# Performance work log

Measured on AMD Instinct MI355X. Metric: run time of the kernel, lower is better.

## Reference

```python
import jax, jax.numpy as jnp
import numpy as np

B, N, D, H, CH = 16, 2048, 2, 128, 32
NEG = -1e9


def setup_inputs() -> dict:
    key = jax.random.key(0)
    ks = jax.random.split(key, 24)
    u = lambda k, shape, fan_in: jax.random.uniform(k, shape, jnp.float32,
                                                    -1.0 / np.sqrt(fan_in), 1.0 / np.sqrt(fan_in))
    inp = {
        "features": jax.random.normal(ks[0], (B, N, D), jnp.float32),
        "adj": jax.random.randint(ks[1], (B, N, N), 0, 2, jnp.int32),
        "candidates": jax.random.randint(ks[2], (B, N), 0, 2, jnp.int32).at[:, 0].set(1),
        "action": jnp.zeros((B,), jnp.int32),
        # GCN encoder (3 layers)
        "W1": u(ks[3], (D, H), D), "b1": jnp.zeros((H,), jnp.float32),
        "W2": u(ks[4], (H, H), H), "b2": jnp.zeros((H,), jnp.float32),
        "W3": u(ks[5], (H, H), H), "b3": jnp.zeros((H,), jnp.float32),
        # learned machine state
        "machine_state": jax.random.uniform(ks[6], (H,), jnp.float32, -1.0, 1.0),
        # actor MLP: Linear(3H,H) -> ReLU -> Linear(H,H) -> ReLU -> Linear(H,1)
        "A1": u(ks[7], (3 * H, H), 3 * H), "ab1": u(ks[8], (H,), 3 * H),
        "A2": u(ks[9], (H, H), H), "ab2": u(ks[10], (H,), H),
        "A3": u(ks[11], (H, 1), H), "ab3": u(ks[12], (1,), H),
        # critic MLP: Linear(H,CH) -> ReLU -> Linear(CH,1)
        "C1": u(ks[13], (H, CH), H), "cb1": u(ks[14], (CH,), H),
        "C2": u(ks[15], (CH, 1), CH), "cb2": u(ks[16], (1,), CH),
    }
    return inp


def _gcn_propagation_matrix(adj):
    # Faithful to PyG GCNConv(add_self_loops=True) fed edges from dense_to_sparse
    # with edge attrs discarded (all weights 1).
    A = (adj != 0).astype(jnp.float32)                      # (B,N,N), A[b,j,i]: edge j->i
    A = jnp.maximum(A, jnp.eye(N, dtype=jnp.float32))       # add_remaining_self_loops
    deg = A.sum(axis=1)                                     # (B,N) incoming degree per target i
    dis = jax.lax.rsqrt(deg)                                # deg >= 1 due to self loops
    # S[b,j,i] = dis[j] * A[j,i] * dis[i]
    return dis[:, :, None] * A * dis[:, None, :]


def reference(features, adj, candidates, action,
              W1, b1, W2, b2, W3, b3, machine_state,
              A1, ab1, A2, ab2, A3, ab3, C1, cb1, C2, cb2):
    S = _gcn_propagation_matrix(adj)
    h = features
    for W, b in ((W1, b1), (W2, b2), (W3, b3)):
        # out[b,i,:] = sum_j S[b,j,i] * (h W)[b,j,:]
        h = jax.nn.relu(jnp.einsum('bji,bjd->bid', S, h @ W) + b)
    pool = h.mean(axis=1)                                   # (B,H) global mean pool

    concat = jnp.concatenate(
        [h,
         jnp.broadcast_to(pool[:, None, :], h.shape),
         jnp.broadcast_to(machine_state[None, None, :], h.shape)], axis=-1)  # (B,N,3H)
    a = jax.nn.relu(concat @ A1 + ab1)
    a = jax.nn.relu(a @ A2 + ab2)
    scores = ((a @ A3 + ab3)[..., 0]) * 10.0                # (B,N)

    probs_sm = jax.nn.softmax(scores, axis=1)               # softmax over jobs
    logits = jnp.where(candidates != 0, probs_sm, NEG)      # masked_fill(~candidates, -inf)
    logp = jax.nn.log_softmax(logits, axis=1)               # Categorical(logits=...)
    log_prob = jnp.take_along_axis(logp, action[:, None].astype(jnp.int32), axis=1)[:, 0]
    p = jnp.exp(logp)
    entropy = -(p * logp).sum(axis=1)

    value = jax.nn.relu(pool @ C1 + cb1) @ C2 + cb2         # (B,1)
    return action, log_prob, entropy, value
```

## Files before the change

### kernel.cpp

```cpp
#include <hip/hip_runtime.h>
#include <hip/hip_bf16.h>
#include <stdint.h>

#define B_  16
#define N_  2048
#define D_  2
#define H_  128
#define CH_ 32
#define NEG_ (-1e9f)

typedef __attribute__((ext_vector_type(8))) short bf16x8;
typedef __attribute__((ext_vector_type(4))) float f32x4;
typedef __attribute__((ext_vector_type(4))) int   v4i;
typedef unsigned short u16;
typedef signed char    i8;

__device__ inline u16 f2bf(float f){
    union { __hip_bfloat16 h; u16 u; } cv;
    cv.h = __float2bfloat16(f);
    return cv.u;
}
__device__ inline float bf2f(u16 v){ return __uint_as_float(((unsigned)v) << 16); }

__device__ inline void gld16b(const void* g, void* l){
    __builtin_amdgcn_global_load_lds(
        (const __attribute__((address_space(1))) unsigned int*)g,
        (__attribute__((address_space(3))) unsigned int*)l, 16, 0, 0);
}

__device__ inline float wredS(float v){
    #pragma unroll
    for (int o = 32; o; o >>= 1) v += __shfl_xor(v, o, 64);
    return v;
}
__device__ inline float wredM(float v){
    #pragma unroll
    for (int o = 32; o; o >>= 1) v = fmaxf(v, __shfl_xor(v, o, 64));
    return v;
}

__global__ __launch_bounds__(256) void k_prep(const int* __restrict__ adj,
                                              i8* __restrict__ ATi8,
                                              float* __restrict__ degF){
    int i0 = blockIdx.x * 64, j0 = blockIdx.y * 64, b = blockIdx.z;
    __shared__ i8 tile[64 * 80];
    __shared__ float degP[256];
    int t = threadIdx.x;
    const int* ap = adj + (size_t)b * N_ * N_;
    #pragma unroll
    for (int it = 0; it < 4; ++it){
        int jj = it * 16 + (t >> 4);
        int gi0 = (t & 15) * 4;
        int4 a4 = *(const int4*)&ap[(size_t)(j0 + jj) * N_ + i0 + gi0];
        int gj = j0 + jj;
        tile[(gi0 + 0) * 80 + jj] = (a4.x != 0 || gj == i0 + gi0 + 0) ? 1 : 0;
        tile[(gi0 + 1) * 80 + jj] = (a4.y != 0 || gj == i0 + gi0 + 1) ? 1 : 0;
        tile[(gi0 + 2) * 80 + jj] = (a4.z != 0 || gj == i0 + gi0 + 2) ? 1 : 0;
        tile[(gi0 + 3) * 80 + jj] = (a4.w != 0 || gj == i0 + gi0 + 3) ? 1 : 0;
    }
    __syncthreads();
    {
        int ii = t & 63, q = t >> 6;
        float s = 0.f;
        #pragma unroll
        for (int k = 0; k < 16; ++k) s += (float)tile[ii * 80 + q * 16 + k];
        degP[t] = s;
    }
    __syncthreads();
    if (t < 64){
        float s = degP[t] + degP[t + 64] + degP[t + 128] + degP[t + 192];
        atomicAdd(&degF[b * N_ + i0 + t], s);
    }
    i8* op = ATi8 + (size_t)b * N_ * N_;
    {
        int io = t >> 2, slot = (t & 3) * 16;
        *(uint4*)&op[(size_t)(i0 + io) * N_ + j0 + slot] = *(const uint4*)&tile[io * 80 + slot];
    }
}

__global__ __launch_bounds__(256) void k_misc(const float* __restrict__ degF,
                                              float* __restrict__ dis,
                                              const float* __restrict__ W2, u16* __restrict__ WT2,
                                              const float* __restrict__ W3, u16* __restrict__ WT3,
                                              const float* __restrict__ A1, u16* __restrict__ A1aT,
                                              const float* __restrict__ A2, u16* __restrict__ A2T){
    int bx = blockIdx.x;
    if (bx < 128){
        int i = bx * 256 + threadIdx.x;
        dis[i] = rsqrtf(degF[i]);
        return;
    }
    int q = (bx - 128) >> 6;
    const float* s; u16* d;
    switch (q){
        case 0: s = W2; d = WT2; break;
        case 1: s = W3; d = WT3; break;
        case 2: s = A1; d = A1aT; break;
        default: s = A2; d = A2T; break;
    }
    int idx = ((bx - 128) & 63) * 256 + threadIdx.x;
    int hp = idx >> 7, k = idx & 127;
    d[hp * 128 + k] = f2bf(s[k * 128 + hp]);
}

__global__ __launch_bounds__(256) void k_y1(const float* __restrict__ feat,
                                            const float* __restrict__ W1,
                                            const float* __restrict__ dis,
                                            u16* __restrict__ YT,
                                            int* __restrict__ absm){
    int t = threadIdx.x;
    int j = blockIdx.x * 256 + t;
    int hg = blockIdx.y * 8;
    int b = blockIdx.z;
    float f0 = feat[((size_t)b * N_ + j) * D_ + 0];
    float f1 = feat[((size_t)b * N_ + j) * D_ + 1];
    float dsc = dis[b * N_ + j];
    float lm = 0.f;
    #pragma unroll
    for (int hh = 0; hh < 8; ++hh){
        int h = hg + hh;
        float v = dsc * (f0 * W1[h] + f1 * W1[H_ + h]);
        lm = fmaxf(lm, fabsf(v));
        YT[(size_t)b * H_ * N_ + (size_t)h * N_ + j] = f2bf(v);
    }
    __shared__ float rmax[256];
    rmax[t] = lm;
    __syncthreads();
    if (t < 128) rmax[t] = fmaxf(rmax[t], rmax[t + 128]);
    __syncthreads();
    if (t < 64){
        float mv = wredM(fmaxf(rmax[t], rmax[t + 64]));
        if (t == 0) atomicMax(&absm[b], __float_as_int(mv));
    }
}

__global__ __launch_bounds__(256) void k_quant(const u16* __restrict__ Yb,
                                               const int* __restrict__ absm,
                                               i8* __restrict__ Yq){
    int idx = (blockIdx.x * 256 + threadIdx.x) * 8;
    int b = idx >> 18;
    float am = __int_as_float(absm[b]);
    float s = (am > 0.f) ? 126.f / am : 0.f;
    bf16x8 y = *(const bf16x8*)&Yb[idx];
    int q[8];
    #pragma unroll
    for (int e = 0; e < 8; ++e){
        float f = bf2f((u16)y[e]) * s;
        q[e] = (int)rintf(f);
    }
    unsigned lo = (q[0] & 255) | ((q[1] & 255) << 8) | ((q[2] & 255) << 16) | ((unsigned)(q[3] & 255) << 24);
    unsigned hi = (q[4] & 255) | ((q[5] & 255) << 8) | ((q[6] & 255) << 16) | ((unsigned)(q[7] & 255) << 24);
    *(uint2*)&Yq[idx] = make_uint2(lo, hi);
}

template<int MODE>
__global__ __launch_bounds__(256, 2) void k_layer(const i8* __restrict__ ATi8,
                                                  const i8* __restrict__ Yq,
                                                  const float* __restrict__ dis,
                                                  const float* __restrict__ bias,
                                                  const int* __restrict__ absmIn,
                                                  const u16* __restrict__ WT,
                                                  u16* __restrict__ Yout,
                                                  int* __restrict__ absmOut,
                                                  u16* __restrict__ h3,
                                                  float* __restrict__ poolF){
    int bid = blockIdx.x;
    int b = bid & 15, i0 = (bid >> 4) * 64;
    const i8* Ab = ATi8 + (size_t)b * N_ * N_ + (size_t)i0 * N_;
    const i8* Bb = Yq   + (size_t)b * H_ * N_;
    __shared__ __align__(16) i8 As[64 * 64];
    __shared__ __align__(16) i8 Bs[128 * 64];
    __shared__ __align__(16) u16 Hs[64 * 136];
    __shared__ __align__(16) u16 Ws[MODE == 0 ? 128 * 136 : 16];
    __shared__ float pmax[256];
    int t = threadIdx.x, w = t >> 6, lane = t & 63, quad = lane >> 4, l16 = lane & 15;
    int mr = w & 1, nc = w >> 1;

    float am = __int_as_float(absmIn[b]);
    float inv_s = am * (1.f / 126.f);

    if (MODE == 0){
        #pragma unroll
        for (int it = 0; it < 8; ++it){
            int e = it * 256 + t;
            int row = e >> 4, c8 = e & 15;
            *(uint4*)&Ws[row * 136 + c8 * 8] = *(const uint4*)&WT[row * 128 + c8 * 8];
        }
    }

    v4i acc[2][4];
    #pragma unroll
    for (int mt = 0; mt < 2; ++mt)
        #pragma unroll
        for (int nt = 0; nt < 4; ++nt) acc[mt][nt] = (v4i){0, 0, 0, 0};

    int srow = lane & 15;
    int sslot = ((lane >> 4) ^ (lane & 3)) * 16;
    int fxo = (quad ^ (l16 & 3)) * 256 + l16 * 16;

    for (int k0 = 0; k0 < N_; k0 += 64){
        #pragma unroll
        for (int it = 0; it < 3; ++it){
            int g = w * 3 + it;
            if (g < 4)
                gld16b(Ab + (size_t)(g * 16 + srow) * N_ + k0 + sslot, As + g * 1024);
            else
                gld16b(Bb + (size_t)((g - 4) * 16 + srow) * N_ + k0 + sslot, Bs + (g - 4) * 1024);
        }
        __syncthreads();
        v4i af[2];
        #pragma unroll
        for (int mt = 0; mt < 2; ++mt)
            af[mt] = *(const v4i*)&As[(mr * 2 + mt) * 1024 + fxo];
        #pragma unroll
        for (int nt = 0; nt < 4; ++nt){
            v4i bv = *(const v4i*)&Bs[(nc * 4 + nt) * 1024 + fxo];
            #pragma unroll
            for (int mt = 0; mt < 2; ++mt)
                acc[mt][nt] = __builtin_amdgcn_mfma_i32_16x16x64_i8(af[mt], bv, acc[mt][nt], 0, 0, 0);
        }
        __syncthreads();
    }

    #pragma unroll
    for (int mt = 0; mt < 2; ++mt)
        #pragma unroll
        for (int r = 0; r < 4; ++r){
            int m = mr * 32 + mt * 16 + quad * 4 + r;
            float dsc = dis[b * N_ + i0 + m];
            #pragma unroll
            for (int nt = 0; nt < 4; ++nt){
                int n = nc * 64 + nt * 16 + l16;
                float v = dsc * ((float)acc[mt][nt][r] * inv_s) + bias[n];
                Hs[m * 136 + n] = f2bf(v > 0.f ? v : 0.f);
            }
        }
    __syncthreads();

    if (MODE == 0){
        f32x4 a2[2][4];
        #pragma unroll
        for (int mt = 0; mt < 2; ++mt)
            #pragma unroll
            for (int nt = 0; nt < 4; ++nt) a2[mt][nt] = (f32x4){0.f, 0.f, 0.f, 0.f};
        #pragma unroll
        for (int kc = 0; kc < 4; ++kc){
            bf16x8 af[2];
            #pragma unroll
            for (int mt = 0; mt < 2; ++mt)
                af[mt] = *(const bf16x8*)&Hs[(mr * 32 + mt * 16 + l16) * 136 + kc * 32 + quad * 8];
            #pragma unroll
            for (int nt = 0; nt < 4; ++nt){
                bf16x8 bv = *(const bf16x8*)&Ws[(nc * 64 + nt * 16 + l16) * 136 + kc * 32 + quad * 8];
                #pragma unroll
                for (int mt = 0; mt < 2; ++mt)
                    a2[mt][nt] = __builtin_amdgcn_mfma_f32_16x16x32_bf16(af[mt], bv, a2[mt][nt], 0, 0, 0);
            }
        }
        __syncthreads();
        float lmax = 0.f;
        #pragma unroll
        for (int mt = 0; mt < 2; ++mt)
            #pragma unroll
            for (int r = 0; r < 4; ++r){
                int m = mr * 32 + mt * 16 + quad * 4 + r;
                float dsc = dis[b * N_ + i0 + m];
                #pragma unroll
                for (int nt = 0; nt < 4; ++nt){
                    float v = dsc * a2[mt][nt][r];
                    lmax = fmaxf(lmax, fabsf(v));
                    Hs[m * 136 + nc * 64 + nt * 16 + l16] = f2bf(v);
                }
            }
        pmax[t] = lmax;
        __syncthreads();
        size_t obase = (size_t)b * H_ * N_ + i0;
        int j = t & 63, hq = t >> 6;
        #pragma unroll 8
        for (int rep = 0; rep < 32; ++rep){
            int hrow = hq * 32 + rep;
            Yout[obase + (size_t)hrow * N_ + j] = Hs[j * 136 + hrow];
        }
        if (t < 64){
            float mv = fmaxf(fmaxf(pmax[t], pmax[t + 64]), fmaxf(pmax[t + 128], pmax[t + 192]));
            mv = wredM(mv);
            if (t == 0) atomicMax(&absmOut[b], __float_as_int(mv));
        }
    } else {
        #pragma unroll
        for (int rep = 0; rep < 4; ++rep){
            int e = rep * 256 + t;
            int row = e >> 4, c8 = e & 15;
            *(uint4*)&h3[((size_t)b * N_ + i0 + row) * H_ + c8 * 8] = *(const uint4*)&Hs[row * 136 + c8 * 8];
        }
        int n = t & 127, rq = t >> 7;
        float ps = 0.f;
        #pragma unroll 8
        for (int r = 0; r < 32; ++r) ps += bf2f(Hs[(rq * 32 + r) * 136 + n]);
        pmax[t] = ps;
        __syncthreads();
        if (t < 128)
            atomicAdd(&poolF[b * H_ + t], (pmax[t] + pmax[t + 128]) * (1.f / N_));
    }
}

__global__ __launch_bounds__(256) void k_cv(const float* __restrict__ poolF,
                                            const float* __restrict__ ms,
                                            const float* __restrict__ A1,
                                            const float* __restrict__ ab1,
                                            const float* __restrict__ C1,
                                            const float* __restrict__ cb1,
                                            const float* __restrict__ C2,
                                            const float* __restrict__ cb2,
                                            float* __restrict__ cvec,
                                            float* __restrict__ out){
    int b = blockIdx.x, t = threadIdx.x;
    __shared__ float pl[128], msl[128], v1[32];
    if (t < 128){ pl[t] = poolF[b * H_ + t]; msl[t] = ms[t]; }
    __syncthreads();
    if (t < 128){
        float c = ab1[t];
        for (int k = 0; k < 128; ++k)
            c += pl[k] * A1[(128 + k) * H_ + t] + msl[k] * A1[(256 + k) * H_ + t];
        cvec[b * H_ + t] = c;
    } else if (t < 160){
        int cc = t - 128;
        float v = cb1[cc];
        for (int k = 0; k < 128; ++k) v += pl[k] * C1[k * CH_ + cc];
        v1[cc] = v > 0.f ? v : 0.f;
    }
    __syncthreads();
    if (t == 0){
        float v = cb2[0];
        for (int c = 0; c < CH_; ++c) v += v1[c] * C2[c];
        out[48 + b] = v;
    }
}

__global__ __launch_bounds__(256) void k_actor(const u16* __restrict__ h3,
                                               const u16* __restrict__ A1aT,
                                               const u16* __restrict__ A2T,
                                               const float* __restrict__ cvec,
                                               const float* __restrict__ ab2,
                                               const float* __restrict__ A3,
                                               const float* __restrict__ ab3,
                                               float* __restrict__ scores){
    int b = blockIdx.x, i0 = blockIdx.y * 128;
    const u16* Ab = h3 + ((size_t)b * N_ + i0) * H_;
    __shared__ __align__(16) u16 As[128 * 72];
    __shared__ __align__(16) u16 Bs[128 * 72];
    __shared__ __align__(16) u16 M1[128 * 136];
    __shared__ float sLDS[128];
    int t = threadIdx.x, w = t >> 6, lane = t & 63, quad = lane >> 4, l16 = lane & 15;
    int sr = t >> 3, sc = (t & 7) * 8;
    f32x4 acc[2][8];
    #pragma unroll
    for (int mt = 0; mt < 2; ++mt)
        #pragma unroll
        for (int nt = 0; nt < 8; ++nt) acc[mt][nt] = (f32x4){0.f, 0.f, 0.f, 0.f};
    for (int k0 = 0; k0 < H_; k0 += 64){
        #pragma unroll
        for (int it = 0; it < 4; ++it){
            int r = sr + it * 32;
            *(uint4*)&As[r * 72 + sc] = *(const uint4*)&Ab[(size_t)r * H_ + k0 + sc];
            *(uint4*)&Bs[r * 72 + sc] = *(const uint4*)&A1aT[(size_t)r * H_ + k0 + sc];
        }
        __syncthreads();
        #pragma unroll
        for (int kc = 0; kc < 2; ++kc){
            bf16x8 af[2];
            #pragma unroll
            for (int mt = 0; mt < 2; ++mt)
                af[mt] = *(const bf16x8*)&As[(w * 32 + mt * 16 + l16) * 72 + kc * 32 + quad * 8];
            #pragma unroll
            for (int nt = 0; nt < 8; ++nt){
                bf16x8 bfr = *(const bf16x8*)&Bs[(nt * 16 + l16) * 72 + kc * 32 + quad * 8];
                #pragma unroll
                for (int mt = 0; mt < 2; ++mt)
                    acc[mt][nt] = __builtin_amdgcn_mfma_f32_16x16x32_bf16(af[mt], bfr, acc[mt][nt], 0, 0, 0);
            }
        }
        __syncthreads();
    }
    const float* cv = cvec + b * H_;
    #pragma unroll
    for (int mt = 0; mt < 2; ++mt)
        #pragma unroll
        for (int r = 0; r < 4; ++r){
            int m = w * 32 + mt * 16 + quad * 4 + r;
            #pragma unroll
            for (int nt = 0; nt < 8; ++nt){
                int n = nt * 16 + l16;
                float v = acc[mt][nt][r] + cv[n];
                M1[m * 136 + n] = f2bf(v > 0.f ? v : 0.f);
                acc[mt][nt][r] = 0.f;
            }
        }
    if (t < 128) sLDS[t] = 0.f;
    for (int k0 = 0; k0 < H_; k0 += 64){
        #pragma unroll
        for (int it = 0; it < 4; ++it){
            int r = sr + it * 32;
            *(uint4*)&Bs[r * 72 + sc] = *(const uint4*)&A2T[(size_t)r * H_ + k0 + sc];
        }
        __syncthreads();
        #pragma unroll
        for (int kc = 0; kc < 2; ++kc){
            bf16x8 af[2];
            #pragma unroll
            for (int mt = 0; mt < 2; ++mt)
                af[mt] = *(const bf16x8*)&M1[(w * 32 + mt * 16 + l16) * 136 + k0 + kc * 32 + quad * 8];
            #pragma unroll
            for (int nt = 0; nt < 8; ++nt){
                bf16x8 bfr = *(const bf16x8*)&Bs[(nt * 16 + l16) * 72 + kc * 32 + quad * 8];
                #pragma unroll
                for (int mt = 0; mt < 2; ++mt)
                    acc[mt][nt] = __builtin_amdgcn_mfma_f32_16x16x32_bf16(af[mt], bfr, acc[mt][nt], 0, 0, 0);
            }
        }
        __syncthreads();
    }
    #pragma unroll
    for (int mt = 0; mt < 2; ++mt)
        #pragma unroll
        for (int r = 0; r < 4; ++r){
            int m = w * 32 + mt * 16 + quad * 4 + r;
            float part = 0.f;
            #pragma unroll
            for (int nt = 0; nt < 8; ++nt){
                int n = nt * 16 + l16;
                float v = acc[mt][nt][r] + ab2[n];
                v = v > 0.f ? v : 0.f;
                part += v * A3[n];
            }
            atomicAdd(&sLDS[m], part);
        }
    __syncthreads();
    if (t < 128) scores[(size_t)b * N_ + i0 + t] = (sLDS[t] + ab3[0]) * 10.f;
}

__global__ __launch_bounds__(256) void k_sm(const float* __restrict__ scores,
                                            const int* __restrict__ cand,
                                            const int* __restrict__ action,
                                            float* __restrict__ out){
    int b = blockIdx.x, t = threadIdx.x;
    __shared__ float sc[N_];
    __shared__ float red[4];
    __shared__ float lps;
    const float* sp = scores + (size_t)b * N_;
    const int*   cp = cand   + (size_t)b * N_;
    float mx = -1e30f;
    for (int i = t; i < N_; i += 256){ float v = sp[i]; sc[i] = v; mx = fmaxf(mx, v); }
    mx = wredM(mx);
    if ((t & 63) == 0) red[t >> 6] = mx;
    __syncthreads();
    mx = fmaxf(fmaxf(red[0], red[1]), fmaxf(red[2], red[3]));
    __syncthreads();
    float se = 0.f;
    for (int i = t; i < N_; i += 256) se += expf(sc[i] - mx);
    se = wredS(se);
    if ((t & 63) == 0) red[t >> 6] = se;
    __syncthreads();
    float s1 = red[0] + red[1] + red[2] + red[3];
    __syncthreads();
    float inv = 1.f / s1;
    float m2 = -1e30f;
    for (int i = t; i < N_; i += 256){
        float p = expf(sc[i] - mx) * inv;
        sc[i] = p;
        if (cp[i] != 0) m2 = fmaxf(m2, p);
    }
    m2 = wredM(m2);
    if ((t & 63) == 0) red[t >> 6] = m2;
    __syncthreads();
    m2 = fmaxf(fmaxf(red[0], red[1]), fmaxf(red[2], red[3]));
    __syncthreads();
    float s2 = 0.f;
    for (int i = t; i < N_; i += 256) if (cp[i] != 0) s2 += expf(sc[i] - m2);
    s2 = wredS(s2);
    if ((t & 63) == 0) red[t >> 6] = s2;
    __syncthreads();
    float lse = m2 + logf(red[0] + red[1] + red[2] + red[3]);
    __syncthreads();
    int a = action[b];
    float ent = 0.f;
    for (int i = t; i < N_; i += 256){
        float lp = (cp[i] != 0 ? sc[i] : NEG_) - lse;
        float pe = expf(lp);
        ent -= pe * lp;
        if (i == a) lps = lp;
    }
    ent = wredS(ent);
    if ((t & 63) == 0) red[t >> 6] = ent;
    __syncthreads();
    if (t == 0){
        out[b]      = (float)a;
        out[16 + b] = lps;
        out[32 + b] = red[0] + red[1] + red[2] + red[3];
    }
}

extern "C" void kernel_launch(void* const* d_in, const int* in_sizes, int n_in,
                              void* d_out, int out_size, void* d_ws, size_t ws_size,
                              hipStream_t stream) {
    const float* feat = (const float*)d_in[0];
    const int*   adj  = (const int*)d_in[1];
    const int*   cand = (const int*)d_in[2];
    const int*   act  = (const int*)d_in[3];
    const float* W1   = (const float*)d_in[4];
    const float* b1   = (const float*)d_in[5];
    const float* W2   = (const float*)d_in[6];
    const float* b2   = (const float*)d_in[7];
    const float* W3   = (const float*)d_in[8];
    const float* b3   = (const float*)d_in[9];
    const float* ms   = (const float*)d_in[10];
    const float* A1   = (const float*)d_in[11];
    const float* ab1  = (const float*)d_in[12];
    const float* A2   = (const float*)d_in[13];
    const float* ab2  = (const float*)d_in[14];
    const float* A3   = (const float*)d_in[15];
    const float* ab3  = (const float*)d_in[16];
    const float* C1   = (const float*)d_in[17];
    const float* cb1  = (const float*)d_in[18];
    const float* C2   = (const float*)d_in[19];
    const float* cb2  = (const float*)d_in[20];
    float* out = (float*)d_out;

    char* w8 = (char*)d_ws;
    size_t off = 0;
    auto alloc = [&](size_t bytes){ void* p = w8 + off; off += (bytes + 255) & ~(size_t)255; return p; };
    i8*    ATi8  = (i8*)   alloc((size_t)B_ * N_ * N_);
    u16*   Yb16  = (u16*)  alloc((size_t)B_ * H_ * N_ * 2);
    i8*    Yi8A  = (i8*)   alloc((size_t)B_ * H_ * N_);
    i8*    Yi8B  = (i8*)   alloc((size_t)B_ * H_ * N_);
    u16*   hbuf  = (u16*)  alloc((size_t)B_ * N_ * H_ * 2);
    float* degF  = (float*)alloc((size_t)B_ * N_ * 4);
    float* poolF = (float*)alloc((size_t)B_ * H_ * 4);
    int*   absm  = (int*)  alloc(48 * 4);
    float* dis   = (float*)alloc((size_t)B_ * N_ * 4);
    float* cvec  = (float*)alloc((size_t)B_ * H_ * 4);
    float* scr   = (float*)alloc((size_t)B_ * N_ * 4);
    u16*   WT2   = (u16*)  alloc((size_t)H_ * H_ * 2);
    u16*   WT3   = (u16*)  alloc((size_t)H_ * H_ * 2);
    u16*   A1aT  = (u16*)  alloc((size_t)H_ * H_ * 2);
    u16*   A2T   = (u16*)  alloc((size_t)H_ * H_ * 2);

    hipMemsetAsync(degF, 0, (size_t)B_ * N_ * 4 + (size_t)B_ * H_ * 4 + 256, stream);

    k_prep<<<dim3(32, 32, 16), 256, 0, stream>>>(adj, ATi8, degF);
    k_misc<<<dim3(384), 256, 0, stream>>>(degF, dis, W2, WT2, W3, WT3, A1, A1aT, A2, A2T);
    k_y1  <<<dim3(8, 16, 16), 256, 0, stream>>>(feat, W1, dis, Yb16, absm + 0);
    k_quant<<<dim3(2048), 256, 0, stream>>>(Yb16, absm + 0, Yi8A);

    k_layer<0><<<dim3(512), 256, 0, stream>>>(ATi8, Yi8A, dis, b1, absm + 0,  WT2, Yb16, absm + 16, nullptr, nullptr);
    k_quant<<<dim3(2048), 256, 0, stream>>>(Yb16, absm + 16, Yi8B);
    k_layer<0><<<dim3(512), 256, 0, stream>>>(ATi8, Yi8B, dis, b2, absm + 16, WT3, Yb16, absm + 32, nullptr, nullptr);
    k_quant<<<dim3(2048), 256, 0, stream>>>(Yb16, absm + 32, Yi8A);
    k_layer<1><<<dim3(512), 256, 0, stream>>>(ATi8, Yi8A, dis, b3, absm + 32, nullptr, nullptr, nullptr, hbuf, poolF);

    k_cv  <<<dim3(16), 256, 0, stream>>>(poolF, ms, A1, ab1, C1, cb1, C2, cb2, cvec, out);
    k_actor<<<dim3(16, 16), 256, 0, stream>>>(hbuf, A1aT, A2T, cvec, ab2, A3, ab3, scr);
    k_sm  <<<dim3(16), 256, 0, stream>>>(scr, cand, act, out);
}
```

Baseline: 561.7 us.

## Fuse post-prep pipeline into one cooperative persistent kernel with grid syncs

Replaces the chain of separate launches after adjacency prep with a single cooperative kernel that runs every stage in phases separated by grid.sync, with a multi-launch fallback if the cooperative launch fails. Layer-1 input is now quantized directly with per-channel analytic bounds computed from feature maxima, which removes the bf16 intermediate and one quant pass. The separate dis buffer is dropped in favor of recomputing rsqrt(deg), and the second linear reads its weights straight from global memory instead of staging them in shared memory. The aim is to remove launch gaps and small kernels, at the cost of grid-sync overhead and possibly lower occupancy or weaker data reuse in the layer GEMM.

```diff
diff --git a/kernel.cpp b/kernel.cpp
--- a/kernel.cpp
+++ b/kernel.cpp
@@ -1,6 +1,9 @@
 #include <hip/hip_runtime.h>
 #include <hip/hip_bf16.h>
+#include <hip/hip_cooperative_groups.h>
 #include <stdint.h>
+
+namespace cg = cooperative_groups;
 
 #define B_  16
 #define N_  2048
@@ -78,115 +81,108 @@
     }
 }
 
-__global__ __launch_bounds__(256) void k_misc(const float* __restrict__ degF,
-                                              float* __restrict__ dis,
-                                              const float* __restrict__ W2, u16* __restrict__ WT2,
-                                              const float* __restrict__ W3, u16* __restrict__ WT3,
-                                              const float* __restrict__ A1, u16* __restrict__ A1aT,
-                                              const float* __restrict__ A2, u16* __restrict__ A2T){
-    int bx = blockIdx.x;
-    if (bx < 128){
-        int i = bx * 256 + threadIdx.x;
-        dis[i] = rsqrtf(degF[i]);
-        return;
-    }
-    int q = (bx - 128) >> 6;
-    const float* s; u16* d;
-    switch (q){
-        case 0: s = W2; d = WT2; break;
-        case 1: s = W3; d = WT3; break;
-        case 2: s = A1; d = A1aT; break;
-        default: s = A2; d = A2T; break;
-    }
-    int idx = ((bx - 128) & 63) * 256 + threadIdx.x;
-    int hp = idx >> 7, k = idx & 127;
-    d[hp * 128 + k] = f2bf(s[k * 128 + hp]);
-}
-
-__global__ __launch_bounds__(256) void k_y1(const float* __restrict__ feat,
-                                            const float* __restrict__ W1,
-                                            const float* __restrict__ dis,
-                                            u16* __restrict__ YT,
-                                            int* __restrict__ absm){
-    int t = threadIdx.x;
-    int j = blockIdx.x * 256 + t;
-    int hg = blockIdx.y * 8;
-    int b = blockIdx.z;
-    float f0 = feat[((size_t)b * N_ + j) * D_ + 0];
-    float f1 = feat[((size_t)b * N_ + j) * D_ + 1];
-    float dsc = dis[b * N_ + j];
-    float lm = 0.f;
-    #pragma unroll
-    for (int hh = 0; hh < 8; ++hh){
-        int h = hg + hh;
-        float v = dsc * (f0 * W1[h] + f1 * W1[H_ + h]);
-        lm = fmaxf(lm, fabsf(v));
-        YT[(size_t)b * H_ * N_ + (size_t)h * N_ + j] = f2bf(v);
-    }
-    __shared__ float rmax[256];
-    rmax[t] = lm;
-    __syncthreads();
-    if (t < 128) rmax[t] = fmaxf(rmax[t], rmax[t + 128]);
-    __syncthreads();
-    if (t < 64){
-        float mv = wredM(fmaxf(rmax[t], rmax[t + 64]));
-        if (t == 0) atomicMax(&absm[b], __float_as_int(mv));
-    }
-}
-
-__global__ __launch_bounds__(256) void k_quant(const u16* __restrict__ Yb,
-                                               const int* __restrict__ absm,
-                                               i8* __restrict__ Yq){
-    int idx = (blockIdx.x * 256 + threadIdx.x) * 8;
-    int b = idx >> 18;
-    float am = __int_as_float(absm[b]);
-    float s = (am > 0.f) ? 126.f / am : 0.f;
-    bf16x8 y = *(const bf16x8*)&Yb[idx];
-    int q[8];
-    #pragma unroll
-    for (int e = 0; e < 8; ++e){
-        float f = bf2f((u16)y[e]) * s;
-        q[e] = (int)rintf(f);
-    }
-    unsigned lo = (q[0] & 255) | ((q[1] & 255) << 8) | ((q[2] & 255) << 16) | ((unsigned)(q[3] & 255) << 24);
-    unsigned hi = (q[4] & 255) | ((q[5] & 255) << 8) | ((q[6] & 255) << 16) | ((unsigned)(q[7] & 255) << 24);
-    *(uint2*)&Yq[idx] = make_uint2(lo, hi);
-}
-
-template<int MODE>
-__global__ __launch_bounds__(256, 2) void k_layer(const i8* __restrict__ ATi8,
-                                                  const i8* __restrict__ Yq,
-                                                  const float* __restrict__ dis,
-                                                  const float* __restrict__ bias,
-                                                  const int* __restrict__ absmIn,
-                                                  const u16* __restrict__ WT,
-                                                  u16* __restrict__ Yout,
-                                                  int* __restrict__ absmOut,
-                                                  u16* __restrict__ h3,
-                                                  float* __restrict__ poolF){
-    int bid = blockIdx.x;
-    int b = bid & 15, i0 = (bid >> 4) * 64;
-    const i8* Ab = ATi8 + (size_t)b * N_ * N_ + (size_t)i0 * N_;
-    const i8* Bb = Yq   + (size_t)b * H_ * N_;
-    __shared__ __align__(16) i8 As[64 * 64];
-    __shared__ __align__(16) i8 Bs[128 * 64];
-    __shared__ __align__(16) u16 Hs[64 * 136];
-    __shared__ __align__(16) u16 Ws[MODE == 0 ? 128 * 136 : 16];
-    __shared__ float pmax[256];
-    int t = threadIdx.x, w = t >> 6, lane = t & 63, quad = lane >> 4, l16 = lane & 15;
+struct MegaArgs {
+    const float *feat; const int *cand; const int *act;
+    const float *W1, *b1, *W2, *b2, *W3, *b3, *ms;
+    const float *A1, *ab1, *A2, *ab2, *A3, *ab3;
+    const float *C1, *cb1, *C2, *cb2;
+    const i8 *ATi8;
+    float *degF, *poolF; int *absm;
+    float *m01, *invs1, *cvec, *scr;
+    u16 *Yb16, *hbuf, *WT2, *WT3, *A1aT, *A2T;
+    i8 *Yq1, *Yq2;
+    float *out;
+};
+
+__device__ void dev_p1(const MegaArgs& a, int bx, int t, char* smem){
+    if (bx < 16){
+        int b = bx;
+        float lm0 = 0.f, lm1 = 0.f;
+        #pragma unroll
+        for (int it = 0; it < 8; ++it){
+            int j = it * 256 + t;
+            float dsj = rsqrtf(a.degF[b * N_ + j]);
+            lm0 = fmaxf(lm0, dsj * fabsf(a.feat[((size_t)b * N_ + j) * 2 + 0]));
+            lm1 = fmaxf(lm1, dsj * fabsf(a.feat[((size_t)b * N_ + j) * 2 + 1]));
+        }
+        float* r0 = (float*)smem;
+        float* r1 = (float*)(smem + 1024);
+        r0[t] = lm0; r1[t] = lm1;
+        __syncthreads();
+        if (t < 128){ r0[t] = fmaxf(r0[t], r0[t + 128]); r1[t] = fmaxf(r1[t], r1[t + 128]); }
+        __syncthreads();
+        if (t < 64){
+            float m0 = wredM(fmaxf(r0[t], r0[t + 64]));
+            float m1 = wredM(fmaxf(r1[t], r1[t + 64]));
+            if (t == 0){ a.m01[b * 2] = m0; a.m01[b * 2 + 1] = m1; }
+        }
+        __syncthreads();
+    } else if (bx < 272){
+        int q = (bx - 16) >> 6;
+        const float* s; u16* d;
+        switch (q){
+            case 0: s = a.W2; d = a.WT2; break;
+            case 1: s = a.W3; d = a.WT3; break;
+            case 2: s = a.A1; d = a.A1aT; break;
+            default: s = a.A2; d = a.A2T; break;
+        }
+        int idx = ((bx - 16) & 63) * 256 + t;
+        int hp = idx >> 7, k = idx & 127;
+        d[hp * 128 + k] = f2bf(s[k * 128 + hp]);
+    }
+}
+
+__device__ void dev_y1q(const MegaArgs& a, int vb, int t){
+    int b = vb & 15, seg = vb >> 4;
+    float m0 = a.m01[b * 2], m1 = a.m01[b * 2 + 1];
+    int j0 = t * 8;
+    float4 f4[4];
+    #pragma unroll
+    for (int k = 0; k < 4; ++k)
+        f4[k] = *(const float4*)&a.feat[((size_t)b * N_ + j0) * 2 + k * 4];
+    const float* ff = (const float*)f4;
+    float dsj[8];
+    #pragma unroll
+    for (int e = 0; e < 8; ++e) dsj[e] = rsqrtf(a.degF[b * N_ + j0 + e]);
+    #pragma unroll
+    for (int hh = 0; hh < 4; ++hh){
+        int h = seg * 4 + hh;
+        float w0 = a.W1[h], w1 = a.W1[H_ + h];
+        float bound = m0 * fabsf(w0) + m1 * fabsf(w1);
+        float s = (bound > 0.f) ? 126.f / bound : 0.f;
+        if (t == 0) a.invs1[b * H_ + h] = bound * (1.f / 126.f);
+        int q[8];
+        #pragma unroll
+        for (int e = 0; e < 8; ++e){
+            float v = dsj[e] * (ff[2 * e] * w0 + ff[2 * e + 1] * w1);
+            q[e] = (int)rintf(v * s);
+        }
+        unsigned lo = (q[0] & 255) | ((q[1] & 255) << 8) | ((q[2] & 255) << 16) | ((unsigned)(q[3] & 255) << 24);
+        unsigned hi = (q[4] & 255) | ((q[5] & 255) << 8) | ((q[6] & 255) << 16) | ((unsigned)(q[7] & 255) << 24);
+        *(uint2*)&a.Yq1[(size_t)b * H_ * N_ + (size_t)h * N_ + j0] = make_uint2(lo, hi);
+    }
+}
+
+template<int PER_N, int MODE>
+__device__ void layer_phase(const MegaArgs& a, int vbid, int t,
+                            const i8* __restrict__ Yq,
+                            const float* __restrict__ bias,
+                            const int* __restrict__ absmIn,
+                            const u16* __restrict__ WTg,
+                            u16* __restrict__ Yout, int* __restrict__ absmBase,
+                            char* smem){
+    int b = vbid & 15, i0 = (vbid >> 4) * 64;
+    const i8* Ab = a.ATi8 + (size_t)b * N_ * N_ + (size_t)i0 * N_;
+    const i8* Bb = Yq + (size_t)b * H_ * N_;
+    i8*  As = (i8*)smem;
+    i8*  Bs = (i8*)(smem + 4096);
+    u16* Hs = (u16*)(smem + 12288);
+    float* pmax = (float*)(smem + 29696);
+    int w = t >> 6, lane = t & 63, quad = lane >> 4, l16 = lane & 15;
     int mr = w & 1, nc = w >> 1;
 
-    float am = __int_as_float(absmIn[b]);
-    float inv_s = am * (1.f / 126.f);
-
-    if (MODE == 0){
-        #pragma unroll
-        for (int it = 0; it < 8; ++it){
-            int e = it * 256 + t;
-            int row = e >> 4, c8 = e & 15;
-            *(uint4*)&Ws[row * 136 + c8 * 8] = *(const uint4*)&WT[row * 128 + c8 * 8];
-        }
-    }
+    float inv_s = PER_N ? 0.f : __int_as_float(absmIn[b]) * (1.f / 126.f);
+    const float* invN = PER_N ? (a.invs1 + b * H_) : nullptr;
 
     v4i acc[2][4];
     #pragma unroll
@@ -227,11 +223,12 @@
         #pragma unroll
         for (int r = 0; r < 4; ++r){
             int m = mr * 32 + mt * 16 + quad * 4 + r;
-            float dsc = dis[b * N_ + i0 + m];
+            float dsc = rsqrtf(a.degF[b * N_ + i0 + m]);
             #pragma unroll
             for (int nt = 0; nt < 4; ++nt){
                 int n = nc * 64 + nt * 16 + l16;
-                float v = dsc * ((float)acc[mt][nt][r] * inv_s) + bias[n];
+                float z = (float)acc[mt][nt][r] * (PER_N ? invN[n] : inv_s);
+                float v = dsc * z + bias[n];
                 Hs[m * 136 + n] = f2bf(v > 0.f ? v : 0.f);
             }
         }
@@ -251,7 +248,7 @@
                 af[mt] = *(const bf16x8*)&Hs[(mr * 32 + mt * 16 + l16) * 136 + kc * 32 + quad * 8];
             #pragma unroll
             for (int nt = 0; nt < 4; ++nt){
-                bf16x8 bv = *(const bf16x8*)&Ws[(nc * 64 + nt * 16 + l16) * 136 + kc * 32 + quad * 8];
+                bf16x8 bv = *(const bf16x8*)&WTg[(size_t)(nc * 64 + nt * 16 + l16) * H_ + kc * 32 + quad * 8];
                 #pragma unroll
                 for (int mt = 0; mt < 2; ++mt)
                     a2[mt][nt] = __builtin_amdgcn_mfma_f32_16x16x32_bf16(af[mt], bv, a2[mt][nt], 0, 0, 0);
@@ -264,7 +261,7 @@
             #pragma unroll
             for (int r = 0; r < 4; ++r){
                 int m = mr * 32 + mt * 16 + quad * 4 + r;
-                float dsc = dis[b * N_ + i0 + m];
+                float dsc = rsqrtf(a.degF[b * N_ + i0 + m]);
                 #pragma unroll
                 for (int nt = 0; nt < 4; ++nt){
                     float v = dsc * a2[mt][nt][r];
@@ -284,14 +281,14 @@
         if (t < 64){
             float mv = fmaxf(fmaxf(pmax[t], pmax[t + 64]), fmaxf(pmax[t + 128], pmax[t + 192]));
             mv = wredM(mv);
-            if (t == 0) atomicMax(&absmOut[b], __float_as_int(mv));
+            if (t == 0) atomicMax(absmBase + b, __float_as_int(mv));
         }
     } else {
         #pragma unroll
         for (int rep = 0; rep < 4; ++rep){
             int e = rep * 256 + t;
             int row = e >> 4, c8 = e & 15;
-            *(uint4*)&h3[((size_t)b * N_ + i0 + row) * H_ + c8 * 8] = *(const uint4*)&Hs[row * 136 + c8 * 8];
+            *(uint4*)&a.hbuf[((size_t)b * N_ + i0 + row) * H_ + c8 * 8] = *(const uint4*)&Hs[row * 136 + c8 * 8];
         }
         int n = t & 127, rq = t >> 7;
         float ps = 0.f;
@@ -300,155 +297,120 @@
         pmax[t] = ps;
         __syncthreads();
         if (t < 128)
-            atomicAdd(&poolF[b * H_ + t], (pmax[t] + pmax[t + 128]) * (1.f / N_));
-    }
-}
-
-__global__ __launch_bounds__(256) void k_cv(const float* __restrict__ poolF,
-                                            const float* __restrict__ ms,
-                                            const float* __restrict__ A1,
-                                            const float* __restrict__ ab1,
-                                            const float* __restrict__ C1,
-                                            const float* __restrict__ cb1,
-                                            const float* __restrict__ C2,
-                                            const float* __restrict__ cb2,
-                                            float* __restrict__ cvec,
-                                            float* __restrict__ out){
-    int b = blockIdx.x, t = threadIdx.x;
-    __shared__ float pl[128], msl[128], v1[32];
-    if (t < 128){ pl[t] = poolF[b * H_ + t]; msl[t] = ms[t]; }
+            atomicAdd(&a.poolF[b * H_ + t], (pmax[t] + pmax[t + 128]) * (1.f / N_));
+    }
+    __syncthreads();
+}
+
+__device__ void dev_quant(const MegaArgs& a, int stage, int vb, int t){
+    const int* am = a.absm + stage * 16;
+    i8* dst = stage ? a.Yq1 : a.Yq2;
+    int idx = vb * 256 + t;
+    #pragma unroll
+    for (int it = 0; it < 4; ++it){
+        int pos = (it * 131072 + idx) * 8;
+        int b = pos >> 18;
+        float m = __int_as_float(am[b]);
+        float s = (m > 0.f) ? 126.f / m : 0.f;
+        bf16x8 y = *(const bf16x8*)&a.Yb16[pos];
+        int q[8];
+        #pragma unroll
+        for (int e = 0; e < 8; ++e) q[e] = (int)rintf(bf2f((u16)y[e]) * s);
+        unsigned lo = (q[0] & 255) | ((q[1] & 255) << 8) | ((q[2] & 255) << 16) | ((unsigned)(q[3] & 255) << 24);
+        unsigned hi = (q[4] & 255) | ((q[5] & 255) << 8) | ((q[6] & 255) << 16) | ((unsigned)(q[7] & 255) << 24);
+        *(uint2*)&dst[pos] = make_uint2(lo, hi);
+    }
+}
+
+__device__ void dev_cv(const MegaArgs& a, int b, int t, char* smem){
+    float* pl  = (float*)smem;
+    float* msl = (float*)(smem + 512);
+    float* v1  = (float*)(smem + 1024);
+    if (t < 128){ pl[t] = a.poolF[b * H_ + t]; msl[t] = a.ms[t]; }
     __syncthreads();
     if (t < 128){
-        float c = ab1[t];
+        float c = a.ab1[t];
         for (int k = 0; k < 128; ++k)
-            c += pl[k] * A1[(128 + k) * H_ + t] + msl[k] * A1[(256 + k) * H_ + t];
-        cvec[b * H_ + t] = c;
+            c += pl[k] * a.A1[(128 + k) * H_ + t] + msl[k] * a.A1[(256 + k) * H_ + t];
+        a.cvec[b * H_ + t] = c;
     } else if (t < 160){
         int cc = t - 128;
-        float v = cb1[cc];
-        for (int k = 0; k < 128; ++k) v += pl[k] * C1[k * CH_ + cc];
+        float v = a.cb1[cc];
+        for (int k = 0; k < 128; ++k) v += pl[k] * a.C1[k * CH_ + cc];
         v1[cc] = v > 0.f ? v : 0.f;
     }
     __syncthreads();
     if (t == 0){
-        float v = cb2[0];
-        for (int c = 0; c < CH_; ++c) v += v1[c] * C2[c];
-        out[48 + b] = v;
-    }
-}
-
-__global__ __launch_bounds__(256) void k_actor(const u16* __restrict__ h3,
-                                               const u16* __restrict__ A1aT,
-                                               const u16* __restrict__ A2T,
-                                               const float* __restrict__ cvec,
-                                               const float* __restrict__ ab2,
-                                               const float* __restrict__ A3,
-                                               const float* __restrict__ ab3,
-                                               float* __restrict__ scores){
-    int b = blockIdx.x, i0 = blockIdx.y * 128;
-    const u16* Ab = h3 + ((size_t)b * N_ + i0) * H_;
-    __shared__ __align__(16) u16 As[128 * 72];
-    __shared__ __align__(16) u16 Bs[128 * 72];
-    __shared__ __align__(16) u16 M1[128 * 136];
-    __shared__ float sLDS[128];
-    int t = threadIdx.x, w = t >> 6, lane = t & 63, quad = lane >> 4, l16 = lane & 15;
-    int sr = t >> 3, sc = (t & 7) * 8;
-    f32x4 acc[2][8];
-    #pragma unroll
-    for (int mt = 0; mt < 2; ++mt)
-        #pragma unroll
-        for (int nt = 0; nt < 8; ++nt) acc[mt][nt] = (f32x4){0.f, 0.f, 0.f, 0.f};
-    for (int k0 = 0; k0 < H_; k0 += 64){
-        #pragma unroll
-        for (int it = 0; it < 4; ++it){
-            int r = sr + it * 32;
-            *(uint4*)&As[r * 72 + sc] = *(const uint4*)&Ab[(size_t)r * H_ + k0 + sc];
-            *(uint4*)&Bs[r * 72 + sc] = *(const uint4*)&A1aT[(size_t)r * H_ + k0 + sc];
-        }
-        __syncthreads();
-        #pragma unroll
-        for (int kc = 0; kc < 2; ++kc){
-            bf16x8 af[2];
-            #pragma unroll
-            for (int mt = 0; mt < 2; ++mt)
-                af[mt] = *(const bf16x8*)&As[(w * 32 + mt * 16 + l16) * 72 + kc * 32 + quad * 8];
-            #pragma unroll
-            for (int nt = 0; nt < 8; ++nt){
-                bf16x8 bfr = *(const bf16x8*)&Bs[(nt * 16 + l16) * 72 + kc * 32 + quad * 8];
-                #pragma unroll
-                for (int mt = 0; mt < 2; ++mt)
-                    acc[mt][nt] = __builtin_amdgcn_mfma_f32_16x16x32_bf16(af[mt], bfr, acc[mt][nt], 0, 0, 0);
-            }
-        }
-        __syncthreads();
-    }
-    const float* cv = cvec + b * H_;
-    #pragma unroll
-    for (int mt = 0; mt < 2; ++mt)
-        #pragma unroll
-        for (int r = 0; r < 4; ++r){
-            int m = w * 32 + mt * 16 + quad * 4 + r;
-            #pragma unroll
-            for (int nt = 0; nt < 8; ++nt){
-                int n = nt * 16 + l16;
-                float v = acc[mt][nt][r] + cv[n];
-                M1[m * 136 + n] = f2bf(v > 0.f ? v : 0.f);
-                acc[mt][nt][r] = 0.f;
-            }
-        }
-    if (t < 128) sLDS[t] = 0.f;
-    for (int k0 = 0; k0 < H_; k0 += 64){
-        #pragma unroll
-        for (int it = 0; it < 4; ++it){
-            int r = sr + it * 32;
-            *(uint4*)&Bs[r * 72 + sc] = *(const uint4*)&A2T[(size_t)r * H_ + k0 + sc];
-        }
-        __syncthreads();
-        #pragma unroll
-        for (int kc = 0; kc < 2; ++kc){
-            bf16x8 af[2];
-            #pragma unroll
-            for (int mt = 0; mt < 2; ++mt)
-                af[mt] = *(const bf16x8*)&M1[(w * 32 + mt * 16 + l16) * 136 + k0 + kc * 32 + quad * 8];
-            #pragma unroll
-            for (int nt = 0; nt < 8; ++nt){
-                bf16x8 bfr = *(const bf16x8*)&Bs[(nt * 16 + l16) * 72 + kc * 32 + quad * 8];
-                #pragma unroll
-                for (int mt = 0; mt < 2; ++mt)
-                    acc[mt][nt] = __builtin_amdgcn_mfma_f32_16x16x32_bf16(af[mt], bfr, acc[mt][nt], 0, 0, 0);
-            }
-        }
-        __syncthreads();
-    }
-    #pragma unroll
-    for (int mt = 0; mt < 2; ++mt)
-        #pragma unroll
-        for (int r = 0; r < 4; ++r){
-            int m = w * 32 + mt * 16 + quad * 4 + r;
-            float part = 0.f;
-            #pragma unroll
-            for (int nt = 0; nt < 8; ++nt){
-                int n = nt * 16 + l16;
-                float v = acc[mt][nt][r] + ab2[n];
-                v = v > 0.f ? v : 0.f;
-                part += v * A3[n];
-            }
-            atomicAdd(&sLDS[m], part);
-        }
-    __syncthreads();
-    if (t < 128) scores[(size_t)b * N_ + i0 + t] = (sLDS[t] + ab3[0]) * 10.f;
-}
-
-__global__ __launch_bounds__(256) void k_sm(const float* __restrict__ scores,
-                                            const int* __restrict__ cand,
-                                            const int* __restrict__ action,
-                                            float* __restrict__ out){
-    int b = blockIdx.x, t = threadIdx.x;
-    __shared__ float sc[N_];
-    __shared__ float red[4];
-    __shared__ float lps;
-    const float* sp = scores + (size_t)b * N_;
-    const int*   cp = cand   + (size_t)b * N_;
+        float v = a.cb2[0];
+        for (int c = 0; c < CH_; ++c) v += v1[c] * a.C2[c];
+        a.out[48 + b] = v;
+    }
+    __syncthreads();
+}
+
+__device__ void dev_actor(const MegaArgs& a, int vbid, int t, char* smem){
+    int b = vbid & 15, i0 = (vbid >> 4) * 64;
+    const u16* Ab = a.hbuf + ((size_t)b * N_ + i0) * H_;
+    u16* M1 = (u16*)smem;
+    int w = t >> 6, lane = t & 63, quad = lane >> 4, l16 = lane & 15;
+    f32x4 acc[8];
+    #pragma unroll
+    for (int nt = 0; nt < 8; ++nt) acc[nt] = (f32x4){0.f, 0.f, 0.f, 0.f};
+    #pragma unroll
+    for (int kc = 0; kc < 4; ++kc){
+        bf16x8 af = *(const bf16x8*)&Ab[(size_t)(w * 16 + l16) * H_ + kc * 32 + quad * 8];
+        #pragma unroll
+        for (int nt = 0; nt < 8; ++nt){
+            bf16x8 bv = *(const bf16x8*)&a.A1aT[(size_t)(nt * 16 + l16) * H_ + kc * 32 + quad * 8];
+            acc[nt] = __builtin_amdgcn_mfma_f32_16x16x32_bf16(af, bv, acc[nt], 0, 0, 0);
+        }
+    }
+    const float* cv = a.cvec + b * H_;
+    #pragma unroll
+    for (int r = 0; r < 4; ++r){
+        int m = w * 16 + quad * 4 + r;
+        #pragma unroll
+        for (int nt = 0; nt < 8; ++nt){
+            int n = nt * 16 + l16;
+            float v = acc[nt][r] + cv[n];
+            M1[m * 136 + n] = f2bf(v > 0.f ? v : 0.f);
+            acc[nt][r] = 0.f;
+        }
+    }
+    #pragma unroll
+    for (int kc = 0; kc < 4; ++kc){
+        bf16x8 af = *(const bf16x8*)&M1[(w * 16 + l16) * 136 + kc * 32 + quad * 8];
+        #pragma unroll
+        for (int nt = 0; nt < 8; ++nt){
+            bf16x8 bv = *(const bf16x8*)&a.A2T[(size_t)(nt * 16 + l16) * H_ + kc * 32 + quad * 8];
+            acc[nt] = __builtin_amdgcn_mfma_f32_16x16x32_bf16(af, bv, acc[nt], 0, 0, 0);
+        }
+    }
+    float ab3v = a.ab3[0];
+    #pragma unroll
+    for (int r = 0; r < 4; ++r){
+        int m = w * 16 + quad * 4 + r;
+        float part = 0.f;
+        #pragma unroll
+        for (int nt = 0; nt < 8; ++nt){
+            int n = nt * 16 + l16;
+            float v = acc[nt][r] + a.ab2[n];
+            v = v > 0.f ? v : 0.f;
+            part += v * a.A3[n];
+        }
+        #pragma unroll
+        for (int o = 1; o < 16; o <<= 1) part += __shfl_xor(part, o, 64);
+        if (l16 == 0) a.scr[(size_t)b * N_ + i0 + m] = (part + ab3v) * 10.f;
+    }
+    __syncthreads();
+}
+
+__device__ void dev_sm(const MegaArgs& a, int b, int t, char* smem){
+    float* sc  = (float*)smem;
+    float* red = (float*)(smem + 8192);
+    float* lps = (float*)(smem + 8256);
+    const float* sp = a.scr + (size_t)b * N_;
+    const int*   cp = a.cand + (size_t)b * N_;
     float mx = -1e30f;
     for (int i = t; i < N_; i += 256){ float v = sp[i]; sc[i] = v; mx = fmaxf(mx, v); }
     mx = wredM(mx);
@@ -482,22 +444,87 @@
     __syncthreads();
     float lse = m2 + logf(red[0] + red[1] + red[2] + red[3]);
     __syncthreads();
-    int a = action[b];
+    int ac = a.act[b];
     float ent = 0.f;
     for (int i = t; i < N_; i += 256){
         float lp = (cp[i] != 0 ? sc[i] : NEG_) - lse;
         float pe = expf(lp);
         ent -= pe * lp;
-        if (i == a) lps = lp;
+        if (i == ac) *lps = lp;
     }
     ent = wredS(ent);
     if ((t & 63) == 0) red[t >> 6] = ent;
     __syncthreads();
     if (t == 0){
-        out[b]      = (float)a;
-        out[16 + b] = lps;
-        out[32 + b] = red[0] + red[1] + red[2] + red[3];
-    }
+        a.out[b]      = (float)ac;
+        a.out[16 + b] = *lps;
+        a.out[32 + b] = red[0] + red[1] + red[2] + red[3];
+    }
+}
+
+__global__ __launch_bounds__(256, 2) void k_mega(MegaArgs a){
+    cg::grid_group grid = cg::this_grid();
+    __shared__ __align__(16) char smem[30720];
+    int bid = blockIdx.x, t = threadIdx.x, G = gridDim.x;
+
+    for (int bx = bid; bx < 272; bx += G) dev_p1(a, bx, t, smem);
+    grid.sync();
+    for (int vb = bid; vb < 512; vb += G) dev_y1q(a, vb, t);
+    grid.sync();
+    for (int vb = bid; vb < 512; vb += G)
+        layer_phase<1, 0>(a, vb, t, a.Yq1, a.b1, nullptr, a.WT2, a.Yb16, a.absm, smem);
+    grid.sync();
+    for (int vb = bid; vb < 512; vb += G) dev_quant(a, 0, vb, t);
+    grid.sync();
+    for (int vb = bid; vb < 512; vb += G)
+        layer_phase<0, 0>(a, vb, t, a.Yq2, a.b2, a.absm, a.WT3, a.Yb16, a.absm + 16, smem);
+    grid.sync();
+    for (int vb = bid; vb < 512; vb += G) dev_quant(a, 1, vb, t);
+    grid.sync();
+    for (int vb = bid; vb < 512; vb += G)
+        layer_phase<0, 1>(a, vb, t, a.Yq1, a.b3, a.absm + 16, nullptr, nullptr, nullptr, smem);
+    grid.sync();
+    if (bid < 16) dev_cv(a, bid, t, smem);
+    grid.sync();
+    for (int vb = bid; vb < 512; vb += G) dev_actor(a, vb, t, smem);
+    grid.sync();
+    if (bid < 16) dev_sm(a, bid, t, smem);
+}
+
+__global__ __launch_bounds__(256) void f_p1(MegaArgs a){
+    __shared__ __align__(16) char sm[2048];
+    dev_p1(a, blockIdx.x, threadIdx.x, sm);
+}
+__global__ __launch_bounds__(256) void f_y1q(MegaArgs a){
+    dev_y1q(a, blockIdx.x, threadIdx.x);
+}
+__global__ __launch_bounds__(256, 2) void f_l1(MegaArgs a){
+    __shared__ __align__(16) char sm[30720];
+    layer_phase<1, 0>(a, blockIdx.x, threadIdx.x, a.Yq1, a.b1, nullptr, a.WT2, a.Yb16, a.absm, sm);
+}
+__global__ __launch_bounds__(256, 2) void f_l2(MegaArgs a){
+    __shared__ __align__(16) char sm[30720];
+    layer_phase<0, 0>(a, blockIdx.x, threadIdx.x, a.Yq2, a.b2, a.absm, a.WT3, a.Yb16, a.absm + 16, sm);
+}
+__global__ __launch_bounds__(256, 2) void f_l3(MegaArgs a){
+    __shared__ __align__(16) char sm[30720];
+    layer_phase<0, 1>(a, blockIdx.x, threadIdx.x, a.Yq1, a.b3, a.absm + 16, nullptr, nullptr, nullptr, sm);
+}
+template<int S>
+__global__ __launch_bounds__(256) void f_q(MegaArgs a){
+    dev_quant(a, S, blockIdx.x, threadIdx.x);
+}
+__global__ __launch_bounds__(256) void f_cv(MegaArgs a){
+    __shared__ __align__(16) char sm[2048];
+    dev_cv(a, blockIdx.x, threadIdx.x, sm);
+}
+__global__ __launch_bounds__(256) void f_actor(MegaArgs a){
+    __shared__ __align__(16) char sm[17408];
+    dev_actor(a, blockIdx.x, threadIdx.x, sm);
+}
+__global__ __launch_bounds__(256) void f_sm(MegaArgs a){
+    __shared__ __align__(16) char sm[8320];
+    dev_sm(a, blockIdx.x, threadIdx.x, sm);
 }
 
 extern "C" void kernel_launch(void* const* d_in, const int* in_sizes, int n_in,
@@ -505,39 +532,20 @@
                               hipStream_t stream) {
     const float* feat = (const float*)d_in[0];
     const int*   adj  = (const int*)d_in[1];
-    const int*   cand = (const int*)d_in[2];
-    const int*   act  = (const int*)d_in[3];
-    const float* W1   = (const float*)d_in[4];
-    const float* b1   = (const float*)d_in[5];
-    const float* W2   = (const float*)d_in[6];
-    const float* b2   = (const float*)d_in[7];
-    const float* W3   = (const float*)d_in[8];
-    const float* b3   = (const float*)d_in[9];
-    const float* ms   = (const float*)d_in[10];
-    const float* A1   = (const float*)d_in[11];
-    const float* ab1  = (const float*)d_in[12];
-    const float* A2   = (const float*)d_in[13];
-    const float* ab2  = (const float*)d_in[14];
-    const float* A3   = (const float*)d_in[15];
-    const float* ab3  = (const float*)d_in[16];
-    const float* C1   = (const float*)d_in[17];
-    const float* cb1  = (const float*)d_in[18];
-    const float* C2   = (const float*)d_in[19];
-    const float* cb2  = (const float*)d_in[20];
-    float* out = (float*)d_out;
 
     char* w8 = (char*)d_ws;
     size_t off = 0;
     auto alloc = [&](size_t bytes){ void* p = w8 + off; off += (bytes + 255) & ~(size_t)255; return p; };
     i8*    ATi8  = (i8*)   alloc((size_t)B_ * N_ * N_);
     u16*   Yb16  = (u16*)  alloc((size_t)B_ * H_ * N_ * 2);
-    i8*    Yi8A  = (i8*)   alloc((size_t)B_ * H_ * N_);
-    i8*    Yi8B  = (i8*)   alloc((size_t)B_ * H_ * N_);
+    i8*    Yq1   = (i8*)   alloc((size_t)B_ * H_ * N_);
+    i8*    Yq2   = (i8*)   alloc((size_t)B_ * H_ * N_);
     u16*   hbuf  = (u16*)  alloc((size_t)B_ * N_ * H_ * 2);
     float* degF  = (float*)alloc((size_t)B_ * N_ * 4);
     float* poolF = (float*)alloc((size_t)B_ * H_ * 4);
-    int*   absm  = (int*)  alloc(48 * 4);
-    float* dis   = (float*)alloc((size_t)B_ * N_ * 4);
+    int*   absm  = (int*)  alloc(256);
+    float* m01   = (float*)alloc(32 * 4);
+    float* invs1 = (float*)alloc((size_t)B_ * H_ * 4);
     float* cvec  = (float*)alloc((size_t)B_ * H_ * 4);
     float* scr   = (float*)alloc((size_t)B_ * N_ * 4);
     u16*   WT2   = (u16*)  alloc((size_t)H_ * H_ * 2);
@@ -548,17 +556,43 @@
     hipMemsetAsync(degF, 0, (size_t)B_ * N_ * 4 + (size_t)B_ * H_ * 4 + 256, stream);
 
     k_prep<<<dim3(32, 32, 16), 256, 0, stream>>>(adj, ATi8, degF);
-    k_misc<<<dim3(384), 256, 0, stream>>>(degF, dis, W2, WT2, W3, WT3, A1, A1aT, A2, A2T);
-    k_y1  <<<dim3(8, 16, 16), 256, 0, stream>>>(feat, W1, dis, Yb16, absm + 0);
-    k_quant<<<dim3(2048), 256, 0, stream>>>(Yb16, absm + 0, Yi8A);
-
-    k_layer<0><<<dim3(512), 256, 0, stream>>>(ATi8, Yi8A, dis, b1, absm + 0,  WT2, Yb16, absm + 16, nullptr, nullptr);
-    k_quant<<<dim3(2048), 256, 0, stream>>>(Yb16, absm + 16, Yi8B);
-    k_layer<0><<<dim3(512), 256, 0, stream>>>(ATi8, Yi8B, dis, b2, absm + 16, WT3, Yb16, absm + 32, nullptr, nullptr);
-    k_quant<<<dim3(2048), 256, 0, stream>>>(Yb16, absm + 32, Yi8A);
-    k_layer<1><<<dim3(512), 256, 0, stream>>>(ATi8, Yi8A, dis, b3, absm + 32, nullptr, nullptr, nullptr, hbuf, poolF);
-
-    k_cv  <<<dim3(16), 256, 0, stream>>>(poolF, ms, A1, ab1, C1, cb1, C2, cb2, cvec, out);
-    k_actor<<<dim3(16, 16), 256, 0, stream>>>(hbuf, A1aT, A2T, cvec, ab2, A3, ab3, scr);
-    k_sm  <<<dim3(16), 256, 0, stream>>>(scr, cand, act, out);
-}
+
+    MegaArgs ma;
+    ma.feat = feat; ma.cand = (const int*)d_in[2]; ma.act = (const int*)d_in[3];
+    ma.W1 = (const float*)d_in[4];  ma.b1 = (const float*)d_in[5];
+    ma.W2 = (const float*)d_in[6];  ma.b2 = (const float*)d_in[7];
+    ma.W3 = (const float*)d_in[8];  ma.b3 = (const float*)d_in[9];
+    ma.ms = (const float*)d_in[10];
+    ma.A1 = (const float*)d_in[11]; ma.ab1 = (const float*)d_in[12];
+    ma.A2 = (const float*)d_in[13]; ma.ab2 = (const float*)d_in[14];
+    ma.A3 = (const float*)d_in[15]; ma.ab3 = (const float*)d_in[16];
+    ma.C1 = (const float*)d_in[17]; ma.cb1 = (const float*)d_in[18];
+    ma.C2 = (const float*)d_in[19]; ma.cb2 = (const float*)d_in[20];
+    ma.ATi8 = ATi8; ma.degF = degF; ma.poolF = poolF; ma.absm = absm;
+    ma.m01 = m01; ma.invs1 = invs1; ma.cvec = cvec; ma.scr = scr;
+    ma.Yb16 = Yb16; ma.hbuf = hbuf; ma.WT2 = WT2; ma.WT3 = WT3;
+    ma.A1aT = A1aT; ma.A2T = A2T; ma.Yq1 = Yq1; ma.Yq2 = Yq2;
+    ma.out = (float*)d_out;
+
+    void* params[] = { &ma };
+    hipError_t ce = hipLaunchCooperativeKernel((void*)k_mega, dim3(512), dim3(256),
+                                               params, 0, stream);
+    if (ce != hipSuccess){
+        (void)hipGetLastError();
+        ce = hipLaunchCooperativeKernel((void*)k_mega, dim3(256), dim3(256),
+                                        params, 0, stream);
+    }
+    if (ce != hipSuccess){
+        (void)hipGetLastError();
+        f_p1   <<<dim3(272), 256, 0, stream>>>(ma);
+        f_y1q  <<<dim3(512), 256, 0, stream>>>(ma);
+        f_l1   <<<dim3(512), 256, 0, stream>>>(ma);
+        f_q<0> <<<dim3(512), 256, 0, stream>>>(ma);
+        f_l2   <<<dim3(512), 256, 0, stream>>>(ma);
+        f_q<1> <<<dim3(512), 256, 0, stream>>>(ma);
+        f_l3   <<<dim3(512), 256, 0, stream>>>(ma);
+        f_cv   <<<dim3(16),  256, 0, stream>>>(ma);
+        f_actor<<<dim3(512), 256, 0, stream>>>(ma);
+        f_sm   <<<dim3(16),  256, 0, stream>>>(ma);
+    }
+}
```

After: 1.035 ms. 84.3% more time.
